# Kernel tuning notes

Hardware: AMD Instinct MI355X
Metric: run time of the kernel (lower is better)

Reference implementation:

```python
import jax, jax.numpy as jnp
import numpy as np

B, H = 131072, 768          # batch of CLS vectors, roberta-base hidden size
C_SIZES = (2, 3, 4, 2)      # label_dict['c'] head sizes; offsets [0,2,5,9]


def setup_inputs() -> dict:
    key = jax.random.key(0)
    ks = jax.random.split(key, 14)
    def lin(kw, kb, out_dim):
        W = jax.random.normal(kw, (out_dim, H), jnp.float32) * 0.02
        b = jax.random.normal(kb, (out_dim,), jnp.float32) * 0.02
        return W, b
    x = jax.random.normal(ks[0], (B, H), jnp.float32)
    Wa, ba = lin(ks[1], ks[2], 2)
    Wb, bb = lin(ks[3], ks[4], 4)            # label_dict['b'] - 1 = 4
    Wc1, bc1 = lin(ks[5], ks[6], C_SIZES[0])
    Wc2, bc2 = lin(ks[7], ks[8], C_SIZES[1])
    Wc3, bc3 = lin(ks[9], ks[10], C_SIZES[2])
    Wc4, bc4 = lin(ks[11], ks[12], C_SIZES[3])
    return dict(x=x, Wa=Wa, ba=ba, Wb=Wb, bb=bb,
                Wc1=Wc1, bc1=bc1, Wc2=Wc2, bc2=bc2,
                Wc3=Wc3, bc3=bc3, Wc4=Wc4, bc4=bc4)


def reference(x, Wa, ba, Wb, bb, Wc1, bc1, Wc2, bc2, Wc3, bc3, Wc4, bc4):
    # taskA head (dropout prob = 0.0 -> identity)
    out_a = x @ Wa.T + ba                          # [B, 2]
    pred_a = jnp.argmax(out_a, axis=1)             # per-sample route: 0 -> skip
    active = (pred_a != 0)[:, None]                # [B, 1]

    # taskB head, scattered into out_b[:, 1:] only for active samples
    tb = x @ Wb.T + bb                             # [B, 4]
    out_b = jnp.concatenate(
        [jnp.zeros((x.shape[0], 1), x.dtype), jnp.where(active, tb, 0.0)],
        axis=1)                                    # [B, 5]

    # taskC: taskB argmax selects one of 4 heads; outputs land at fixed
    # contiguous column offsets (get_c_offset) in out_c; inactive -> zeros.
    pred_b = jnp.argmax(tb, axis=1)                # 0..3 -> head '1'..'4'
    parts = []
    for k, (Wc, bc) in enumerate([(Wc1, bc1), (Wc2, bc2), (Wc3, bc3), (Wc4, bc4)]):
        mask = active & (pred_b == k)[:, None]     # this head routed & active
        parts.append(jnp.where(mask, x @ Wc.T + bc, 0.0))
    out_c = jnp.concatenate(parts, axis=1)         # [B, 11]

    return out_a, out_b, out_c
```

## Files before the change

### kernel.cpp

```cpp
#include <hip/hip_runtime.h>

#define HDIM 768

constexpr int KC    = 32;
constexpr int KHALF = HDIM / 2;
constexpr int NCH   = KHALF / KC;
constexpr int RPB   = 128;
constexpr int PITCH = 2 * KC + 4;

#define W_LIST(OP)                                                            \
    OP(0,  Wa,  0) OP(1,  Wa,  1)                                             \
    OP(2,  Wb,  0) OP(3,  Wb,  1) OP(4,  Wb,  2) OP(5,  Wb,  3)               \
    OP(6,  Wc1, 0) OP(7,  Wc1, 1)                                             \
    OP(8,  Wc2, 0) OP(9,  Wc2, 1) OP(10, Wc2, 2)                              \
    OP(11, Wc3, 0) OP(12, Wc3, 1) OP(13, Wc3, 2) OP(14, Wc3, 3)               \
    OP(15, Wc4, 0) OP(16, Wc4, 1)

#define LOADW(j, WP, R) const float4 w##j = *(const float4*)((WP) + (R) * HDIM + kb);

#define FMAW(j, WP, R)                                                        \
    ac0[j] = fmaf(xv0.x, w##j.x, ac0[j]); ac1[j] = fmaf(xv1.x, w##j.x, ac1[j]); \
    ac0[j] = fmaf(xv0.y, w##j.y, ac0[j]); ac1[j] = fmaf(xv1.y, w##j.y, ac1[j]); \
    ac0[j] = fmaf(xv0.z, w##j.z, ac0[j]); ac1[j] = fmaf(xv1.z, w##j.z, ac1[j]); \
    ac0[j] = fmaf(xv0.w, w##j.w, ac0[j]); ac1[j] = fmaf(xv1.w, w##j.w, ac1[j]);

#define WRITE_ROW(ACC, ROW)                                                   \
    do {                                                                      \
        const int row_ = (ROW);                                               \
        if (row_ < B) {                                                       \
            const float oa0 = ACC[0] + ba[0];                                 \
            const float oa1 = ACC[1] + ba[1];                                 \
            const bool active = oa1 > oa0;                                    \
            const float tb0 = ACC[2] + bb[0];                                 \
            const float tb1 = ACC[3] + bb[1];                                 \
            const float tb2 = ACC[4] + bb[2];                                 \
            const float tb3 = ACC[5] + bb[3];                                 \
            int   p = 0;                                                      \
            float m = tb0;                                                    \
            if (tb1 > m) { m = tb1; p = 1; }                                  \
            if (tb2 > m) { m = tb2; p = 2; }                                  \
            if (tb3 > m) { m = tb3; p = 3; }                                  \
            float* oa = out + (size_t)2 * row_;                               \
            oa[0] = oa0;                                                      \
            oa[1] = oa1;                                                      \
            float* ob = out + (size_t)2 * B + (size_t)5 * row_;               \
            ob[0] = 0.f;                                                      \
            ob[1] = active ? tb0 : 0.f;                                       \
            ob[2] = active ? tb1 : 0.f;                                       \
            ob[3] = active ? tb2 : 0.f;                                       \
            ob[4] = active ? tb3 : 0.f;                                       \
            const bool m0 = active && (p == 0);                               \
            const bool m1 = active && (p == 1);                               \
            const bool m2 = active && (p == 2);                               \
            const bool m3 = active && (p == 3);                               \
            float* oc = out + (size_t)7 * B + (size_t)11 * row_;              \
            oc[0]  = m0 ? ACC[6]  + bc1[0] : 0.f;                             \
            oc[1]  = m0 ? ACC[7]  + bc1[1] : 0.f;                             \
            oc[2]  = m1 ? ACC[8]  + bc2[0] : 0.f;                             \
            oc[3]  = m1 ? ACC[9]  + bc2[1] : 0.f;                             \
            oc[4]  = m1 ? ACC[10] + bc2[2] : 0.f;                             \
            oc[5]  = m2 ? ACC[11] + bc3[0] : 0.f;                             \
            oc[6]  = m2 ? ACC[12] + bc3[1] : 0.f;                             \
            oc[7]  = m2 ? ACC[13] + bc3[2] : 0.f;                             \
            oc[8]  = m2 ? ACC[14] + bc3[3] : 0.f;                             \
            oc[9]  = m3 ? ACC[15] + bc4[0] : 0.f;                             \
            oc[10] = m3 ? ACC[16] + bc4[1] : 0.f;                             \
        }                                                                     \
    } while (0)

__global__ __launch_bounds__(128, 2)
void hier_fused(const float* __restrict__ x,
                const float* __restrict__ Wa,  const float* __restrict__ ba,
                const float* __restrict__ Wb,  const float* __restrict__ bb,
                const float* __restrict__ Wc1, const float* __restrict__ bc1,
                const float* __restrict__ Wc2, const float* __restrict__ bc2,
                const float* __restrict__ Wc3, const float* __restrict__ bc3,
                const float* __restrict__ Wc4, const float* __restrict__ bc4,
                float* __restrict__ out, int B)
{
    __shared__ float xs[RPB * PITCH];

    const int t       = threadIdx.x;
    const int rr      = t & 63;
    const int kh      = t >> 6;
    const int rowBase = blockIdx.x * RPB;

    int vz;
    asm("v_mov_b32 %0, 0" : "=v"(vz));

    float ac0[17], ac1[17];
#pragma unroll
    for (int j = 0; j < 17; ++j) { ac0[j] = 0.f; ac1[j] = 0.f; }

    const int col4 = (t & 15) * 4;
    const int grp  = t >> 4;
    const int gOff = (col4 < KC) ? col4
                                 : (KHALF - KC + col4);

    for (int c = 0; c < NCH; ++c) {
        __syncthreads();
        const int gcol = c * KC + gOff;
#pragma unroll
        for (int i = 0; i < 16; ++i) {
            int r2  = grp + i * 8;
            int row = rowBase + r2;
            if (row >= B) row = B - 1;
            const float4 v = *(const float4*)&x[(size_t)row * HDIM + gcol];
            *(float4*)&xs[r2 * PITCH + col4] = v;
        }
        __syncthreads();

        const float* xr0   = &xs[rr * PITCH + kh * KC];
        const float* xr1   = xr0 + 64 * PITCH;
        const int    kbase = kh * KHALF + c * KC + vz;
#pragma unroll 2
        for (int kk = 0; kk < KC; kk += 4) {
            const float4 xv0 = *(const float4*)(xr0 + kk);
            const float4 xv1 = *(const float4*)(xr1 + kk);
            const int kb = kbase + kk;
            W_LIST(LOADW)
            W_LIST(FMAW)
        }
    }

    __syncthreads();
    if (kh == 1) {
#pragma unroll
        for (int j = 0; j < 17; ++j) {
            xs[rr * 19 + j]        = ac0[j];
            xs[(rr + 64) * 19 + j] = ac1[j];
        }
    }
    __syncthreads();
    if (kh != 0) return;

#pragma unroll
    for (int j = 0; j < 17; ++j) {
        ac0[j] += xs[rr * 19 + j];
        ac1[j] += xs[(rr + 64) * 19 + j];
    }

    WRITE_ROW(ac0, rowBase + rr);
    WRITE_ROW(ac1, rowBase + rr + 64);
}

extern "C" void kernel_launch(void* const* d_in, const int* in_sizes, int n_in,
                              void* d_out, int out_size, void* d_ws, size_t ws_size,
                              hipStream_t stream) {
    const float* x   = (const float*)d_in[0];
    const float* Wa  = (const float*)d_in[1];
    const float* ba  = (const float*)d_in[2];
    const float* Wb  = (const float*)d_in[3];
    const float* bb  = (const float*)d_in[4];
    const float* Wc1 = (const float*)d_in[5];
    const float* bc1 = (const float*)d_in[6];
    const float* Wc2 = (const float*)d_in[7];
    const float* bc2 = (const float*)d_in[8];
    const float* Wc3 = (const float*)d_in[9];
    const float* bc3 = (const float*)d_in[10];
    const float* Wc4 = (const float*)d_in[11];
    const float* bc4 = (const float*)d_in[12];

    const int B  = in_sizes[0] / HDIM;
    const int nb = (B + RPB - 1) / RPB;

    hipLaunchKernelGGL(hier_fused, dim3(nb), dim3(128), 0, stream,
                       x, Wa, ba, Wb, bb, Wc1, bc1, Wc2, bc2, Wc3, bc3, Wc4, bc4,
                       (float*)d_out, B);
}
```

Before: 591.2 us.

## Double-buffer x and weight chunks via direct global-to-LDS async loads

```diff
diff --git a/kernel.cpp b/kernel.cpp
--- a/kernel.cpp
+++ b/kernel.cpp
@@ -2,11 +2,16 @@
 
 #define HDIM 768
 
-constexpr int KC    = 32;
+constexpr int KC    = 16;
 constexpr int KHALF = HDIM / 2;
 constexpr int NCH   = KHALF / KC;
 constexpr int RPB   = 128;
-constexpr int PITCH = 2 * KC + 4;
+
+__device__ __forceinline__ void gload_lds16(const float* g, float* l) {
+    __builtin_amdgcn_global_load_lds(
+        (const __attribute__((address_space(1))) unsigned int*)(g),
+        (__attribute__((address_space(3))) unsigned int*)(l), 16, 0, 0);
+}
 
 #define W_LIST(OP)                                                            \
     OP(0,  Wa,  0) OP(1,  Wa,  1)                                             \
@@ -16,7 +21,7 @@
     OP(11, Wc3, 0) OP(12, Wc3, 1) OP(13, Wc3, 2) OP(14, Wc3, 3)               \
     OP(15, Wc4, 0) OP(16, Wc4, 1)
 
-#define LOADW(j, WP, R) const float4 w##j = *(const float4*)((WP) + (R) * HDIM + kb);
+#define LOADW(j, WP, R) const float4 w##j = *(const float4*)(wb + (j) * 32);
 
 #define FMAW(j, WP, R)                                                        \
     ac0[j] = fmaf(xv0.x, w##j.x, ac0[j]); ac1[j] = fmaf(xv1.x, w##j.x, ac1[j]); \
@@ -78,57 +83,75 @@
                 const float* __restrict__ Wc4, const float* __restrict__ bc4,
                 float* __restrict__ out, int B)
 {
-    __shared__ float xs[RPB * PITCH];
+    __shared__ float xs[2][8 * 512];
+    __shared__ float ws[2][544];
 
     const int t       = threadIdx.x;
     const int rr      = t & 63;
     const int kh      = t >> 6;
+    const int wv      = t >> 6;
     const int rowBase = blockIdx.x * RPB;
-
-    int vz;
-    asm("v_mov_b32 %0, 0" : "=v"(vz));
 
     float ac0[17], ac1[17];
 #pragma unroll
     for (int j = 0; j < 17; ++j) { ac0[j] = 0.f; ac1[j] = 0.f; }
 
-    const int col4 = (t & 15) * 4;
-    const int grp  = t >> 4;
-    const int gOff = (col4 < KC) ? col4
-                                 : (KHALF - KC + col4);
+    int srow = rowBase + t; if (srow >= B) srow = B - 1;
+    const float* xsrc = x + (size_t)srow * HDIM;
+
+    const float* wsrc1;
+    {
+        const int h = t >> 3, s = t & 7;
+        const float* base =
+            h < 2  ? Wa  + (size_t)h * HDIM :
+            h < 6  ? Wb  + (size_t)(h - 2) * HDIM :
+            h < 8  ? Wc1 + (size_t)(h - 6) * HDIM :
+            h < 11 ? Wc2 + (size_t)(h - 8) * HDIM :
+            h < 15 ? Wc3 + (size_t)(h - 11) * HDIM :
+                     Wc4 + (size_t)(h - 15) * HDIM;
+        wsrc1 = base + (s < 4 ? s * 4 : KHALF + (s - 4) * 4);
+    }
+    const int s2 = t & 7;
+    const float* wsrc2 = Wc4 + HDIM + (s2 < 4 ? s2 * 4 : KHALF + (s2 - 4) * 4);
+
+#define STAGE(cc)                                                             \
+    do {                                                                      \
+        const int nb_  = (cc) & 1;                                            \
+        const int coff = (cc) * KC;       \
+        _Pragma("unroll")                                                     \
+        for (int j = 0; j < 8; ++j) {                                         \
+            const int go = (j < 4 ? j * 4 : KHALF + (j - 4) * 4) + coff;      \
+            gload_lds16(xsrc + go, &xs[nb_][j * 512 + wv * 256]);             \
+        }                                                                     \
+        gload_lds16(wsrc1 + coff, &ws[nb_][wv * 256]);                        \
+        if (t < 8) gload_lds16(wsrc2 + coff, &ws[nb_][512]);                  \
+    } while (0)
+
+    STAGE(0);
+    __syncthreads();
 
     for (int c = 0; c < NCH; ++c) {
-        __syncthreads();
-        const int gcol = c * KC + gOff;
+        if (c + 1 < NCH) STAGE(c + 1);
+
+        const int cur = c & 1;
+        const float* xbase = &xs[cur][kh * 4 * 512 + rr * 4];
 #pragma unroll
-        for (int i = 0; i < 16; ++i) {
-            int r2  = grp + i * 8;
-            int row = rowBase + r2;
-            if (row >= B) row = B - 1;
-            const float4 v = *(const float4*)&x[(size_t)row * HDIM + gcol];
-            *(float4*)&xs[r2 * PITCH + col4] = v;
-        }
-        __syncthreads();
-
-        const float* xr0   = &xs[rr * PITCH + kh * KC];
-        const float* xr1   = xr0 + 64 * PITCH;
-        const int    kbase = kh * KHALF + c * KC + vz;
-#pragma unroll 2
-        for (int kk = 0; kk < KC; kk += 4) {
-            const float4 xv0 = *(const float4*)(xr0 + kk);
-            const float4 xv1 = *(const float4*)(xr1 + kk);
-            const int kb = kbase + kk;
+        for (int q = 0; q < 4; ++q) {
+            const float4 xv0 = *(const float4*)(xbase + q * 512);
+            const float4 xv1 = *(const float4*)(xbase + q * 512 + 256);
+            const float* wb  = &ws[cur][kh * 16 + q * 4];
             W_LIST(LOADW)
             W_LIST(FMAW)
         }
+        __syncthreads();
     }
+#undef STAGE
 
-    __syncthreads();
     if (kh == 1) {
 #pragma unroll
         for (int j = 0; j < 17; ++j) {
-            xs[rr * 19 + j]        = ac0[j];
-            xs[(rr + 64) * 19 + j] = ac1[j];
+            xs[0][rr * 18 + j]        = ac0[j];
+            xs[0][(rr + 64) * 18 + j] = ac1[j];
         }
     }
     __syncthreads();
@@ -136,8 +159,8 @@
 
 #pragma unroll
     for (int j = 0; j < 17; ++j) {
-        ac0[j] += xs[rr * 19 + j];
-        ac1[j] += xs[(rr + 64) * 19 + j];
+        ac0[j] += xs[0][rr * 18 + j];
+        ac1[j] += xs[0][(rr + 64) * 18 + j];
     }
 
     WRITE_ROW(ac0, rowBase + rr);
```

New measurement: 592.7 us. About the same (+0.3%).
